# Kernel tuning notes

Measured on AMD Instinct MI355X. Metric: run time of the kernel, lower is better.

Reference implementation:

```python
import jax, jax.numpy as jnp
import numpy as np

V, E, H, S, B, T = 32000, 256, 512, 128, 32, 32


def setup_inputs() -> dict:
    key = jax.random.key(0)
    ks = iter(jax.random.split(key, 32))

    def w(shape, s=0.05):
        return jax.random.normal(next(ks), shape, dtype=jnp.float32) * s

    return dict(
        src=jax.random.randint(next(ks), (S, B), 0, V),
        trg=jax.random.randint(next(ks), (T, B), 0, V),
        embed=w((V, E)),
        enc_Wih_f=w((4 * H, E)), enc_Whh_f=w((4 * H, H)), enc_bih_f=w((4 * H,)), enc_bhh_f=w((4 * H,)),
        enc_Wih_b=w((4 * H, E)), enc_Whh_b=w((4 * H, H)), enc_bih_b=w((4 * H,)), enc_bhh_b=w((4 * H,)),
        attn_W=w((H, 2 * H)), attn_b=w((H,)), attn_v=w((H,)),
        dec_Wih0=w((4 * H, H + E)), dec_Whh0=w((4 * H, H)), dec_bih0=w((4 * H,)), dec_bhh0=w((4 * H,)),
        dec_Wih1=w((4 * H, H)), dec_Whh1=w((4 * H, H)), dec_bih1=w((4 * H,)), dec_bhh1=w((4 * H,)),
        out_W=w((V, 2 * H)), out_b=w((V,)),
    )


def _cell(x, h, c, Wih, Whh, bih, bhh):
    # PyTorch LSTM gate order: i, f, g, o
    z = x @ Wih.T + h @ Whh.T + bih + bhh
    i, f, g, o = jnp.split(z, 4, axis=-1)
    c2 = jax.nn.sigmoid(f) * c + jax.nn.sigmoid(i) * jnp.tanh(g)
    h2 = jax.nn.sigmoid(o) * jnp.tanh(c2)
    return h2, c2


def _run_lstm(xs, Wih, Whh, bih, bhh):
    # xs: [S, B, in]; returns outputs [S,B,H], final (h,c)
    h0 = jnp.zeros((xs.shape[1], Whh.shape[1]), xs.dtype)

    def step(carry, x):
        h, c = carry
        h2, c2 = _cell(x, h, c, Wih, Whh, bih, bhh)
        return (h2, c2), h2

    (hT, cT), outs = jax.lax.scan(step, (h0, h0), xs)
    return outs, hT, cT


def _forward(src, trg, embed,
             enc_Wih_f, enc_Whh_f, enc_bih_f, enc_bhh_f,
             enc_Wih_b, enc_Whh_b, enc_bih_b, enc_bhh_b,
             attn_W, attn_b, attn_v,
             dec_Wih0, dec_Whh0, dec_bih0, dec_bhh0,
             dec_Wih1, dec_Whh1, dec_bih1, dec_bhh1,
             out_W, out_b):
    emb_src = embed[src]                                  # [S,B,E]
    # bidirectional 1-layer encoder LSTM
    f_outs, hf, cf = _run_lstm(emb_src, enc_Wih_f, enc_Whh_f, enc_bih_f, enc_bhh_f)
    b_outs, hb, cb = _run_lstm(emb_src[::-1], enc_Wih_b, enc_Whh_b, enc_bih_b, enc_bhh_b)
    enc_out = f_outs + b_outs[::-1]                       # [S,B,H] (sum of directions)
    h = jnp.stack([hf, hb])                               # [2,B,H] -> decoder init state
    c = jnp.stack([cf, cb])
    enc_bsh = enc_out.transpose(1, 0, 2)                  # [B,S,H]

    def dec_step(carry, tok):
        h, c = carry
        emb = embed[tok]                                  # [B,E]
        q = h[-1]                                         # top-layer hidden [B,H]
        qs = jnp.broadcast_to(q[:, None, :], enc_bsh.shape)
        energy = jnp.tanh(jnp.concatenate([qs, enc_bsh], -1) @ attn_W.T + attn_b)  # [B,S,H]
        scores = energy @ attn_v                          # [B,S]
        aw = jax.nn.softmax(scores, axis=1)
        ctx = jnp.einsum('bs,bsh->bh', aw, enc_bsh)       # [B,H]
        x = jnp.concatenate([emb, ctx], -1)               # [B,E+H]
        h0, c0 = _cell(x, h[0], c[0], dec_Wih0, dec_Whh0, dec_bih0, dec_bhh0)
        h1, c1 = _cell(h0, h[1], c[1], dec_Wih1, dec_Whh1, dec_bih1, dec_bhh1)
        logits = jax.nn.log_softmax(
            jnp.concatenate([h1, ctx], -1) @ out_W.T + out_b, axis=-1)             # [B,V]
        return (jnp.stack([h0, h1]), jnp.stack([c0, c1])), logits

    # teacher forcing (ratio=1.0): input at step t is trg[t-1]
    _, outs = jax.lax.scan(dec_step, (h, c), trg[:-1])    # [T-1,B,V]
    outputs = jnp.concatenate(
        [jnp.zeros((1,) + outs.shape[1:], outs.dtype), outs], 0)  # outputs[0]=0 as in torch
    return outputs


def reference(src, trg, embed,
              enc_Wih_f, enc_Whh_f, enc_bih_f, enc_bhh_f,
              enc_Wih_b, enc_Whh_b, enc_bih_b, enc_bhh_b,
              attn_W, attn_b, attn_v,
              dec_Wih0, dec_Whh0, dec_bih0, dec_bhh0,
              dec_Wih1, dec_Whh1, dec_bih1, dec_bhh1,
              out_W, out_b):
    return _forward(src, trg, embed,
                    enc_Wih_f, enc_Whh_f, enc_bih_f, enc_bhh_f,
                    enc_Wih_b, enc_Whh_b, enc_bih_b, enc_bhh_b,
                    attn_W, attn_b, attn_v,
                    dec_Wih0, dec_Whh0, dec_bih0, dec_bhh0,
                    dec_Wih1, dec_Whh1, dec_bih1, dec_bhh1,
                    out_W, out_b)
```

## Files before the change

### kernel.cpp

```cpp
#include <hip/hip_runtime.h>
#include <stdint.h>


using short8 = __attribute__((ext_vector_type(8))) short;
using f32x4  = __attribute__((ext_vector_type(4))) float;
typedef _Float16 half2v __attribute__((ext_vector_type(2)));

__device__ __forceinline__ short f2bf(float x){
  unsigned u = __float_as_uint(x);
  unsigned r = (u + 0x7fffu + ((u >> 16) & 1u)) >> 16;
  return (short)(unsigned short)r;
}
__device__ __forceinline__ unsigned bfpair(float a, float b){
  return (unsigned)(unsigned short)f2bf(a) | ((unsigned)(unsigned short)f2bf(b) << 16);
}
__device__ __forceinline__ float bf2f_lo(unsigned u){ return __uint_as_float(u << 16); }
__device__ __forceinline__ float bf2f_hi(unsigned u){ return __uint_as_float(u & 0xffff0000u); }
__device__ __forceinline__ float sigmf(float x){ return 1.0f/(1.0f + __expf(-x)); }
__device__ __forceinline__ float fast_tanh(float x){
  const float e = __expf(2.0f*x);
  return 1.0f - 2.0f/(e + 1.0f);
}
__device__ __forceinline__ unsigned pack_h2(float a, float b){
  unsigned short ha = __builtin_bit_cast(unsigned short, (_Float16)a);
  unsigned short hb = __builtin_bit_cast(unsigned short, (_Float16)b);
  return (unsigned)ha | ((unsigned)hb << 16);
}
__device__ __forceinline__ float h2lo(unsigned u){ return (float)__builtin_bit_cast(half2v,u)[0]; }
__device__ __forceinline__ float h2hi(unsigned u){ return (float)__builtin_bit_cast(half2v,u)[1]; }
__device__ __forceinline__ float dot2u(unsigned x, unsigned w, float c){
#if __has_builtin(__builtin_amdgcn_fdot2)
  return __builtin_amdgcn_fdot2(__builtin_bit_cast(half2v,x), __builtin_bit_cast(half2v,w), c, false);
#else
  half2v hx = __builtin_bit_cast(half2v,x), hw = __builtin_bit_cast(half2v,w);
  c = fmaf((float)hx[0], (float)hw[0], c);
  c = fmaf((float)hx[1], (float)hw[1], c);
  return c;
#endif
}

__device__ __forceinline__ float4 load_coh_f4(const float* p){
  float4 v;
  asm volatile("global_load_dwordx4 %0, %1, off sc0 sc1\n\ts_waitcnt vmcnt(0)"
               : "=&v"(v) : "v"(p) : "memory");
  return v;
}
__device__ __forceinline__ void store_coh_u32(unsigned* p, unsigned v){
  asm volatile("global_store_dword %0, %1, off sc0 sc1" :: "v"(p), "v"(v) : "memory");
}
__device__ __forceinline__ void store_coh_f32(float* p, float v){
  asm volatile("global_store_dword %0, %1, off sc0 sc1" :: "v"(p), "v"(v) : "memory");
}

__device__ __forceinline__ void wait_cnt(const unsigned* base, unsigned target){
  if (threadIdx.x < 64){
    const bool mine = threadIdx.x < 8;
    const unsigned* p = base + (threadIdx.x << 4);
    for(;;){
      unsigned v = target;
      if (mine)
        asm volatile("global_load_dword %0, %1, off sc0 sc1\n\ts_waitcnt vmcnt(0)"
                     : "=&v"(v) : "v"(p) : "memory");
      if (__all(v >= target)) break;
    }
  }
  __syncthreads();
}
__device__ __forceinline__ void add0(unsigned* slot){
  if (threadIdx.x < 64) asm volatile("s_waitcnt vmcnt(0)" ::: "memory");
  if (threadIdx.x == 0)
    __hip_atomic_fetch_add(slot, 1u, __ATOMIC_RELAXED, __HIP_MEMORY_SCOPE_AGENT);
}

__device__ __forceinline__ void stage8u(const unsigned* src, int bg8, unsigned* lds){
  const unsigned* s0 = src + (size_t)bg8*2048;
  const int f0 = threadIdx.x, f1 = f0 + 256;
  uint4 a, b;
  asm volatile(
    "global_load_dwordx4 %0, %2, off sc0 sc1\n\t"
    "global_load_dwordx4 %1, %3, off sc0 sc1\n\t"
    "s_waitcnt vmcnt(0)"
    : "=&v"(a), "=&v"(b)
    : "v"(s0 + (f0<<2)), "v"(s0 + (f1<<2))
    : "memory");
  { const int row = f0>>6, cu = (f0&63)<<2; *(uint4*)&lds[row*260+cu] = a; }
  { const int row = f1>>6, cu = (f1&63)<<2; *(uint4*)&lds[row*260+cu] = b; }
}

__device__ __forceinline__ float dot512(const unsigned* xrow, const unsigned* w){
  float a = 0.f;
  #pragma unroll 4
  for (int it = 0; it < 16; ++it){
    uint4 x0 = *(const uint4*)(xrow + it*16);
    uint4 x1 = *(const uint4*)(xrow + it*16 + 4);
    uint4 x2 = *(const uint4*)(xrow + it*16 + 8);
    uint4 x3 = *(const uint4*)(xrow + it*16 + 12);
    uint4 w0 = *(const uint4*)(w + it*16);
    uint4 w1 = *(const uint4*)(w + it*16 + 4);
    uint4 w2 = *(const uint4*)(w + it*16 + 8);
    uint4 w3 = *(const uint4*)(w + it*16 + 12);
    a = dot2u(x0.x,w0.x,a); a = dot2u(x0.y,w0.y,a); a = dot2u(x0.z,w0.z,a); a = dot2u(x0.w,w0.w,a);
    a = dot2u(x1.x,w1.x,a); a = dot2u(x1.y,w1.y,a); a = dot2u(x1.z,w1.z,a); a = dot2u(x1.w,w1.w,a);
    a = dot2u(x2.x,w2.x,a); a = dot2u(x2.y,w2.y,a); a = dot2u(x2.z,w2.z,a); a = dot2u(x2.w,w2.w,a);
    a = dot2u(x3.x,w3.x,a); a = dot2u(x3.y,w3.y,a); a = dot2u(x3.z,w3.z,a); a = dot2u(x3.w,w3.w,a);
  }
  return a;
}

__device__ __forceinline__ float2 dot2rows(const unsigned* xrow, const unsigned* wA, const unsigned* wB){
  float a = 0.f, b = 0.f;
  #pragma unroll 8
  for (int it = 0; it < 32; ++it){
    uint4 x0 = *(const uint4*)(xrow + it*8);
    uint4 x1 = *(const uint4*)(xrow + it*8 + 4);
    uint4 a0 = *(const uint4*)(wA + it*8);
    uint4 a1 = *(const uint4*)(wA + it*8 + 4);
    uint4 b0 = *(const uint4*)(wB + it*8);
    uint4 b1 = *(const uint4*)(wB + it*8 + 4);
    a = dot2u(x0.x,a0.x,a); a = dot2u(x0.y,a0.y,a); a = dot2u(x0.z,a0.z,a); a = dot2u(x0.w,a0.w,a);
    a = dot2u(x1.x,a1.x,a); a = dot2u(x1.y,a1.y,a); a = dot2u(x1.z,a1.z,a); a = dot2u(x1.w,a1.w,a);
    b = dot2u(x0.x,b0.x,b); b = dot2u(x0.y,b0.y,b); b = dot2u(x0.z,b0.z,b); b = dot2u(x0.w,b0.w,b);
    b = dot2u(x1.x,b1.x,b); b = dot2u(x1.y,b1.y,b); b = dot2u(x1.w,b1.w,b); b = dot2u(x1.z,b1.z,b);
  }
  return make_float2(a, b);
}

__global__ void k_zero(float* __restrict__ p, int n){
  int i = blockIdx.x*256 + threadIdx.x;
  const int stride = gridDim.x*256;
  for (; i < n; i += stride) p[i] = 0.f;
}

__global__ __launch_bounds__(256) void k_cvt_f16(const float* __restrict__ s, unsigned short* __restrict__ d, int n){
  int i = blockIdx.x*256 + threadIdx.x;
  const int stride = gridDim.x*256;
  for (; i < n; i += stride) d[i] = __builtin_bit_cast(unsigned short, (_Float16)s[i]);
}
__global__ __launch_bounds__(256) void k_cvt_f16_str(const float* __restrict__ s, int lds_, unsigned short* __restrict__ d, int n){
  int i = blockIdx.x*256 + threadIdx.x;
  const int stride = gridDim.x*256;
  for (; i < n; i += stride){
    const int row = i >> 9, c = i & 511;
    d[i] = __builtin_bit_cast(unsigned short, (_Float16)s[(size_t)row*lds_ + c]);
  }
}

__global__ __launch_bounds__(256) void k_gather(
    const int* __restrict__ src, const int* __restrict__ trg,
    const float* __restrict__ embed,
    short* __restrict__ emb_src_bf, short* __restrict__ emb_trg_bf)
{
  const int row = blockIdx.x, tid = threadIdx.x;
  if (row < 4096){
    const int tok = src[row];
    emb_src_bf[(size_t)row*256 + tid] = f2bf(embed[(size_t)tok*256 + tid]);
  } else {
    const int r = row - 4096;
    short v = 0;
    if (r < 992){ const int tok = trg[r]; v = f2bf(embed[(size_t)tok*256 + tid]); }
    emb_trg_bf[(size_t)r*256 + tid] = v;
  }
}

__global__ __launch_bounds__(256) void k_gemm_aw(
    const short* __restrict__ A, int lda,
    const float* __restrict__ W, int ldw,
    float* __restrict__ C, int ldc,
    const float* __restrict__ bias0, const float* __restrict__ bias1,
    int Mvalid, int K, int tmode, short* __restrict__ Cbf)
{
  __shared__ __align__(16) short As[128*32];
  __shared__ __align__(16) short Bs[128*32];
  const int tid = threadIdx.x;
  const int bm = blockIdx.x, bn = blockIdx.y;
  const int w  = tid >> 6,  l  = tid & 63;
  const int wm = w >> 1,    wn = w & 1;
  const int lr = l & 15,    lk = l >> 4;

  const int r0 = tid >> 2;
  const int s0 = (tid & 3) << 3;
  const int r1 = r0 + 64;

  const short* a0 = A + (size_t)(bm*128 + r0)*lda + s0;
  const short* a1 = A + (size_t)(bm*128 + r1)*lda + s0;
  const float* w0 = W + (size_t)(bn*128 + r0)*ldw + s0;
  const float* w1 = W + (size_t)(bn*128 + r1)*ldw + s0;

  const f32x4 zero4 = {0.f,0.f,0.f,0.f};
  f32x4 acc[4][4];
  #pragma unroll
  for (int mi=0;mi<4;mi++){
    #pragma unroll
    for (int ni=0;ni<4;ni++) acc[mi][ni] = zero4;
  }

  for (int k0 = 0; k0 < K; k0 += 32){
    short8 va0 = *(const short8*)(a0 + k0);
    short8 va1 = *(const short8*)(a1 + k0);
    float4 f00 = *(const float4*)(w0 + k0);
    float4 f01 = *(const float4*)(w0 + k0 + 4);
    float4 f10 = *(const float4*)(w1 + k0);
    float4 f11 = *(const float4*)(w1 + k0 + 4);
    short8 vb0, vb1;
    vb0[0]=f2bf(f00.x); vb0[1]=f2bf(f00.y); vb0[2]=f2bf(f00.z); vb0[3]=f2bf(f00.w);
    vb0[4]=f2bf(f01.x); vb0[5]=f2bf(f01.y); vb0[6]=f2bf(f01.z); vb0[7]=f2bf(f01.w);
    vb1[0]=f2bf(f10.x); vb1[1]=f2bf(f10.y); vb1[2]=f2bf(f10.z); vb1[3]=f2bf(f10.w);
    vb1[4]=f2bf(f11.x); vb1[5]=f2bf(f11.y); vb1[6]=f2bf(f11.z); vb1[7]=f2bf(f11.w);

    __syncthreads();
    *((short8*)As + tid)       = va0;
    *((short8*)As + tid + 256) = va1;
    *((short8*)Bs + tid)       = vb0;
    *((short8*)Bs + tid + 256) = vb1;
    __syncthreads();

    short8 af[4], bfr[4];
    #pragma unroll
    for (int mi=0;mi<4;mi++) af[mi]  = *(const short8*)&As[(wm*64 + mi*16 + lr)*32 + (lk<<3)];
    #pragma unroll
    for (int ni=0;ni<4;ni++) bfr[ni] = *(const short8*)&Bs[(wn*64 + ni*16 + lr)*32 + (lk<<3)];
    #pragma unroll
    for (int mi=0;mi<4;mi++){
      #pragma unroll
      for (int ni=0;ni<4;ni++)
        acc[mi][ni] = __builtin_amdgcn_mfma_f32_16x16x32_bf16(af[mi], bfr[ni], acc[mi][ni], 0,0,0);
    }
  }

  #pragma unroll
  for (int mi=0;mi<4;mi++){
    const int rb = bm*128 + wm*64 + mi*16 + (lk<<2);
    #pragma unroll
    for (int ni=0;ni<4;ni++){
      const int col = bn*128 + wn*64 + ni*16 + lr;
      float bv = 0.f;
      if (bias0) bv += bias0[col];
      if (bias1) bv += bias1[col];
      #pragma unroll
      for (int rr=0;rr<4;rr++){
        const int row = rb + rr;
        if (row < Mvalid){
          const float vv = acc[mi][ni][rr] + bv;
          if (Cbf)        Cbf[(size_t)row*ldc + col] = f2bf(vv);
          else if (tmode) C[(size_t)(row>>5)*65536 + (size_t)col*32 + (row&31)] = vv;
          else            C[(size_t)row*ldc + col] = vv;
        }
      }
    }
  }
}

__global__ __launch_bounds__(256,1) void k_enc_persist(
    const float* __restrict__ pre_f, const float* __restrict__ pre_b,
    const unsigned short* __restrict__ WhF, const unsigned short* __restrict__ WhB,
    unsigned* __restrict__ f_outs, unsigned* __restrict__ b_outs,
    float* __restrict__ c_f_out, float* __restrict__ c_b_out,
    unsigned* __restrict__ encCnt)
{
  __shared__ __align__(16) unsigned x_lds[8*260];
  __shared__ float zbuf[64*8];
  const int bid = blockIdx.x, tid = threadIdx.x;
  const int x = bid & 7, m = bid >> 3;
  const int dir = m & 1, bg = (m >> 1) & 3, q = m >> 3;
  const int jb = x*4 + q;
  const float* pre = dir ? pre_b : pre_f;
  const unsigned* Wh = (const unsigned*)(dir ? WhB : WhF);
  unsigned* outs = dir ? b_outs : f_outs;
  float* c_out = dir ? c_b_out : c_f_out;
  unsigned* grp = encCnt + (size_t)(dir*4 + bg)*128;
  unsigned* mycnt = grp + x*16;

  const int bb = tid & 7, rr = tid >> 3;
  const int g = rr >> 3, op = rr & 7;
  const unsigned* wA = Wh + (size_t)(g*512 + jb*16 + 2*op)*256;
  const unsigned* wB = wA + 256;

  const int cp = tid & 7, fb = tid >> 3;
  const int b_out = bg*8 + fb;
  const int k0 = jb*16 + 2*cp;
  float c_a = 0.f, c_b2 = 0.f;

  for (int t = 0; t < 128; ++t){
    float pz[8];
    if (tid < 64){
      const int tt = dir ? (127 - t) : t;
      const float* pt = pre + (size_t)tt*65536;
      #pragma unroll
      for (int gg = 0; gg < 4; ++gg){
        pz[gg]   = pt[(size_t)(gg*512 + k0)*32 + b_out];
        pz[gg+4] = pt[(size_t)(gg*512 + k0 + 1)*32 + b_out];
      }
    }
    if (t){
      wait_cnt(grp, 4u*(unsigned)t);
      stage8u(outs + (size_t)(t-1)*8192, bg, x_lds);
    } else {
      for (int i = tid; i < 8*260; i += 256) x_lds[i] = 0;
    }
    __syncthreads();

    const float2 d = dot2rows(x_lds + bb*260, wA, wB);
    zbuf[(g*16 + 2*op)*8 + bb]   = d.x;
    zbuf[(g*16 + 2*op+1)*8 + bb] = d.y;
    __syncthreads();

    if (tid < 64){
      float za[4], zb[4];
      #pragma unroll
      for (int gg = 0; gg < 4; ++gg){
        za[gg] = pz[gg]   + zbuf[(gg*16 + 2*cp)*8 + fb];
        zb[gg] = pz[gg+4] + zbuf[(gg*16 + 2*cp+1)*8 + fb];
      }
      const float ca = sigmf(za[1])*c_a  + sigmf(za[0])*fast_tanh(za[2]);
      const float cb = sigmf(zb[1])*c_b2 + sigmf(zb[0])*fast_tanh(zb[2]);
      c_a = ca; c_b2 = cb;
      const float ha = sigmf(za[3])*fast_tanh(ca);
      const float hb = sigmf(zb[3])*fast_tanh(cb);
      store_coh_u32(outs + (size_t)t*8192 + (size_t)b_out*256 + (k0>>1), pack_h2(ha, hb));
    }
    add0(mycnt);
  }
  if (tid < 64){
    c_out[b_out*512 + k0]     = c_a;
    c_out[b_out*512 + k0 + 1] = c_b2;
  }
}

__global__ __launch_bounds__(256) void k_sum_enc(
    const unsigned* __restrict__ f_o, const unsigned* __restrict__ b_o,
    unsigned* __restrict__ enc_sum_bf_u)
{
  const int i = blockIdx.x*256 + threadIdx.x;
  const int s = i >> 13, rem = i & 8191;
  const unsigned a = f_o[i], b = b_o[(size_t)(127 - s)*8192 + rem];
  const float lo = h2lo(a) + h2lo(b);
  const float hi = h2hi(a) + h2hi(b);
  enc_sum_bf_u[i] = bfpair(lo, hi);
}

__global__ __launch_bounds__(256,1) void k_dec_persist(
    const float* __restrict__ demb,
    const unsigned short* __restrict__ Wih0h,
    const unsigned short* __restrict__ Whh0h,
    const unsigned short* __restrict__ Wih1h,
    const unsigned short* __restrict__ Whh1h,
    const float* __restrict__ bih1, const float* __restrict__ bhh1,
    const unsigned short* __restrict__ wqh,
    const float* __restrict__ attnV,
    const short* __restrict__ enc_proj_bf,
    const unsigned* __restrict__ enc_sum_u,
    const unsigned* __restrict__ h0i, const unsigned* __restrict__ h1i,
    const float* __restrict__ c0_init, const float* __restrict__ c1_init,
    unsigned* __restrict__ h0buf, unsigned* __restrict__ h1buf,
    unsigned* __restrict__ ctxb,
    float* __restrict__ qsb,
    short* __restrict__ h1ctx,
    unsigned* __restrict__ cE1, unsigned* __restrict__ cE2,
    unsigned* __restrict__ cE3, unsigned* __restrict__ cE4)
{
  __shared__ __align__(16) unsigned x1s[8*260];
  __shared__ __align__(16) unsigned x0s[8*260];
  __shared__ float zfin[32*9];
  __shared__ __align__(16) float q_s[512], v_s[512];
  __shared__ float part[256], aw[128], red[128];

  const int bid = blockIdx.x, tid = threadIdx.x;
  const int x = bid & 7;
  const int bg = (bid >> 3) & 3;
  const int q = bid >> 5;
  const int jb = x*8 + q;

  unsigned* e1 = cE1 + bg*128;
  unsigned* e2 = cE2 + bg*128;
  unsigned* e3 = cE3 + bg*128;
  unsigned* e4 = cE4 + bg*128;

  const int b = tid & 7, r = tid >> 3;
  const int g = r >> 3, o = r & 7;
  const int j_row = g*512 + jb*8 + o;

  const int cp = tid & 3, fb = tid >> 2;
  const int b_out = bg*8 + fb;
  const int k0 = jb*8 + 2*cp;

  const unsigned* Wh0row = (const unsigned*)Whh0h + (size_t)j_row*256;
  const unsigned* Wh1row = (const unsigned*)Whh1h + (size_t)j_row*256;
  const unsigned* Wi0row = (const unsigned*)Wih0h + (size_t)j_row*256;
  const unsigned* Wi1row = (const unsigned*)Wih1h + (size_t)j_row*256;

  float c0a = 0.f, c0b = 0.f, c1a = 0.f, c1b = 0.f;
  float b1a[4], b1b[4];
  if (tid < 32){
    c0a = c0_init[b_out*512 + k0];   c0b = c0_init[b_out*512 + k0 + 1];
    c1a = c1_init[b_out*512 + k0];   c1b = c1_init[b_out*512 + k0 + 1];
    #pragma unroll
    for (int gg=0; gg<4; ++gg){
      b1a[gg] = bih1[gg*512 + k0]     + bhh1[gg*512 + k0];
      b1b[gg] = bih1[gg*512 + k0 + 1] + bhh1[gg*512 + k0 + 1];
    }
  }
  if (bid < 32 && tid < 128) ((float4*)v_s)[tid] = ((const float4*)attnV)[tid];

  float zh0 = 0.f;

  for (int t = 0; t < 31; ++t){
    const float demb_v = demb[(size_t)t*65536 + (size_t)j_row*32 + bg*8 + b];

    if (t){
      wait_cnt(e4, 8u*(unsigned)t);
      stage8u(h1buf + (size_t)(t&1)*8192, bg, x1s);
    } else {
      stage8u(h1i, bg, x1s);
      stage8u(h0i, bg, x0s);
    }
    __syncthreads();
    if (t == 0) zh0 = dot512(x0s + b*260, Wh0row);
    const float zh1 = dot512(x1s + b*260, Wh1row);
    if (tid < 64){
      const int qb = tid >> 3, qcol = jb*8 + (tid & 7);
      const float qv = dot512(x1s + qb*260, (const unsigned*)wqh + (size_t)qcol*256);
      store_coh_f32(qsb + (size_t)(bg*8 + qb)*512 + qcol, qv);
    }
    add0(e1 + x*16);

    if (bid < 32){
      wait_cnt(e1, 8u*(unsigned)(t+1));
      const int ab = bid;
      if (tid < 128) ((float4*)q_s)[tid] = load_coh_f4(qsb + (size_t)ab*512 + (tid<<2));
      __syncthreads();
      {
        const int s = tid >> 1, half = tid & 1;
        const unsigned* ep = (const unsigned*)(enc_proj_bf + ((size_t)(s*32 + ab))*512 + (half << 8));
        const float* qh = q_s + (half << 8);
        const float* vh = v_s + (half << 8);
        float p = 0.f;
        for (int kk = 0; kk < 128; kk += 4){
          uint4 e = *(const uint4*)(ep + kk);
          const int k2 = kk << 1;
          p += fast_tanh(qh[k2+0] + bf2f_lo(e.x)) * vh[k2+0];
          p += fast_tanh(qh[k2+1] + bf2f_hi(e.x)) * vh[k2+1];
          p += fast_tanh(qh[k2+2] + bf2f_lo(e.y)) * vh[k2+2];
          p += fast_tanh(qh[k2+3] + bf2f_hi(e.y)) * vh[k2+3];
          p += fast_tanh(qh[k2+4] + bf2f_lo(e.z)) * vh[k2+4];
          p += fast_tanh(qh[k2+5] + bf2f_hi(e.z)) * vh[k2+5];
          p += fast_tanh(qh[k2+6] + bf2f_lo(e.w)) * vh[k2+6];
          p += fast_tanh(qh[k2+7] + bf2f_hi(e.w)) * vh[k2+7];
        }
        part[tid] = p;
      }
      __syncthreads();
      if (tid < 128){ const float sc = part[2*tid] + part[2*tid+1]; aw[tid] = sc; red[tid] = sc; }
      __syncthreads();
      for (int off = 64; off > 0; off >>= 1){
        if (tid < off) red[tid] = fmaxf(red[tid], red[tid+off]);
        __syncthreads();
      }
      const float mx = red[0];
      __syncthreads();
      if (tid < 128){ const float e = __expf(aw[tid] - mx); aw[tid] = e; red[tid] = e; }
      __syncthreads();
      for (int off = 64; off > 0; off >>= 1){
        if (tid < off) red[tid] += red[tid+off];
        __syncthreads();
      }
      const float inv = 1.0f / red[0];
      if (tid < 128) aw[tid] *= inv;
      __syncthreads();
      if (tid < 64){
        const unsigned* es = enc_sum_u + (size_t)ab*256 + (tid<<2);
        float c0=0,c1=0,c2=0,c3=0,c4=0,c5=0,c6=0,c7=0;
        for (int s2 = 0; s2 < 128; ++s2){
          const float a = aw[s2];
          uint4 u = *(const uint4*)(es + (size_t)s2*8192);
          c0 = fmaf(a, bf2f_lo(u.x), c0); c1 = fmaf(a, bf2f_hi(u.x), c1);
          c2 = fmaf(a, bf2f_lo(u.y), c2); c3 = fmaf(a, bf2f_hi(u.y), c3);
          c4 = fmaf(a, bf2f_lo(u.z), c4); c5 = fmaf(a, bf2f_hi(u.z), c5);
          c6 = fmaf(a, bf2f_lo(u.w), c6); c7 = fmaf(a, bf2f_hi(u.w), c7);
        }
        unsigned* cp4 = ctxb + (size_t)ab*256 + (tid<<2);
        store_coh_u32(cp4+0, pack_h2(c0,c1));
        store_coh_u32(cp4+1, pack_h2(c2,c3));
        store_coh_u32(cp4+2, pack_h2(c4,c5));
        store_coh_u32(cp4+3, pack_h2(c6,c7));
        unsigned* hc = (unsigned*)h1ctx + ((size_t)t*16384 + (size_t)ab*512 + 256 + (tid<<2));
        hc[0] = bfpair(c0,c1); hc[1] = bfpair(c2,c3); hc[2] = bfpair(c4,c5); hc[3] = bfpair(c6,c7);
      }
      add0(e2 + (bid & 7)*16);
    }

    wait_cnt(e2, (unsigned)(t+1));
    stage8u(ctxb, bg, x0s);
    __syncthreads();
    zfin[r*9 + b] = demb_v + dot512(x0s + b*260, Wi0row) + zh0;
    __syncthreads();
    if (tid < 32){
      float za[4], zb[4];
      #pragma unroll
      for (int gg=0; gg<4; ++gg){
        za[gg] = zfin[(gg*8 + 2*cp)*9 + fb];
        zb[gg] = zfin[(gg*8 + 2*cp+1)*9 + fb];
      }
      const float ca = sigmf(za[1])*c0a + sigmf(za[0])*fast_tanh(za[2]);
      const float cb = sigmf(zb[1])*c0b + sigmf(zb[0])*fast_tanh(zb[2]);
      c0a = ca; c0b = cb;
      const float ha = sigmf(za[3])*fast_tanh(ca);
      const float hb = sigmf(zb[3])*fast_tanh(cb);
      store_coh_u32(h0buf + (size_t)((t+1)&1)*8192 + (size_t)b_out*256 + (k0>>1), pack_h2(ha, hb));
    }
    add0(e3 + x*16);

    wait_cnt(e3, 8u*(unsigned)(t+1));
    stage8u(h0buf + (size_t)((t+1)&1)*8192, bg, x1s);
    __syncthreads();
    {
      const float2 d = dot2rows(x1s + b*260, Wi1row, Wh0row);
      zfin[r*9 + b] = d.x + zh1;
      zh0 = d.y;
    }
    __syncthreads();
    if (tid < 32){
      float za[4], zb[4];
      #pragma unroll
      for (int gg=0; gg<4; ++gg){
        za[gg] = b1a[gg] + zfin[(gg*8 + 2*cp)*9 + fb];
        zb[gg] = b1b[gg] + zfin[(gg*8 + 2*cp+1)*9 + fb];
      }
      const float ca = sigmf(za[1])*c1a + sigmf(za[0])*fast_tanh(za[2]);
      const float cb = sigmf(zb[1])*c1b + sigmf(zb[0])*fast_tanh(zb[2]);
      c1a = ca; c1b = cb;
      const float ha = sigmf(za[3])*fast_tanh(ca);
      const float hb = sigmf(zb[3])*fast_tanh(cb);
      store_coh_u32(h1buf + (size_t)((t+1)&1)*8192 + (size_t)b_out*256 + (k0>>1), pack_h2(ha, hb));
      ((unsigned*)h1ctx)[(size_t)t*16384 + (size_t)b_out*512 + (k0>>1)] = bfpair(ha, hb);
    }
    add0(e4 + x*16);
  }
}

__global__ __launch_bounds__(256) void k_logsm(float* __restrict__ out){
  float* row = out + (size_t)blockIdx.x * 32000;
  const int tid = threadIdx.x;
  __shared__ float red[256];
  float s = 0.f;
  for (int i = tid; i < 8000; i += 256){
    const float4 v = ((const float4*)row)[i];
    s += __expf(v.x) + __expf(v.y) + __expf(v.z) + __expf(v.w);
  }
  red[tid] = s; __syncthreads();
  for (int off = 128; off > 0; off >>= 1){
    if (tid < off) red[tid] += red[tid+off];
    __syncthreads();
  }
  const float lse = __logf(red[0]);
  for (int i = tid; i < 8000; i += 256){
    float4 v = ((const float4*)row)[i];
    v.x -= lse; v.y -= lse; v.z -= lse; v.w -= lse;
    ((float4*)row)[i] = v;
  }
}

extern "C" void kernel_launch(void* const* d_in, const int* in_sizes, int n_in,
                              void* d_out, int out_size, void* d_ws, size_t ws_size,
                              hipStream_t stream)
{
  (void)in_sizes; (void)n_in; (void)out_size; (void)ws_size;
  const int*   src   = (const int*)d_in[0];
  const int*   trg   = (const int*)d_in[1];
  const float* embed = (const float*)d_in[2];
  const float* eWihF = (const float*)d_in[3];
  const float* eWhhF = (const float*)d_in[4];
  const float* ebihF = (const float*)d_in[5];
  const float* ebhhF = (const float*)d_in[6];
  const float* eWihB = (const float*)d_in[7];
  const float* eWhhB = (const float*)d_in[8];
  const float* ebihB = (const float*)d_in[9];
  const float* ebhhB = (const float*)d_in[10];
  const float* attnW = (const float*)d_in[11];
  const float* attnB = (const float*)d_in[12];
  const float* attnV = (const float*)d_in[13];
  const float* dWih0 = (const float*)d_in[14];
  const float* dWhh0 = (const float*)d_in[15];
  const float* dbih0 = (const float*)d_in[16];
  const float* dbhh0 = (const float*)d_in[17];
  const float* dWih1 = (const float*)d_in[18];
  const float* dWhh1 = (const float*)d_in[19];
  const float* dbih1 = (const float*)d_in[20];
  const float* dbhh1 = (const float*)d_in[21];
  const float* outW  = (const float*)d_in[22];
  const float* outB  = (const float*)d_in[23];

  float* out = (float*)d_out;
  float* enc_in_f = out;
  float* enc_in_b = out + 8388608;
  short* enc_proj_bf = (short*)(out + 18874368);
  unsigned* f_outs = (unsigned*)(out + 20971520);
  unsigned* b_outs = (unsigned*)(out + 23068672);
  float* demb     = out + 25165824;
  short* emb_src_bf = (short*)(out + 27262976);
  short* emb_trg_bf = (short*)(out + 27787264);
  unsigned* enc_sum_bf_u = (unsigned*)(out + 27918336);
  unsigned short* wqh    = (unsigned short*)(out + 28966912);
  unsigned short* whhF_h = (unsigned short*)(out + 29229056);
  unsigned short* whhB_h = (unsigned short*)(out + 29753344);
  unsigned short* wih0_h = (unsigned short*)(out + 30277632);
  unsigned short* whh0_h = (unsigned short*)(out + 30801920);
  unsigned short* wih1_h = (unsigned short*)(out + 31326208);
  unsigned short* whh1_h = (unsigned short*)(out + 31850496);
  float* qsb            = out + 32374784;

  char* ws = (char*)d_ws;
  short* h1ctx = (short*)ws;
  unsigned* h0buf = (unsigned*)(ws + 2097152);
  unsigned* h1buf = (unsigned*)(ws + 2162688);
  unsigned* ctxb  = (unsigned*)(ws + 2228224);
  float* c_f      = (float*)(ws + 2260992);
  float* c_b      = (float*)(ws + 2326528);
  unsigned* encCnt = (unsigned*)(ws + 2392064);
  unsigned* cE1    = encCnt + 1024;
  unsigned* cE2    = cE1 + 512;
  unsigned* cE3    = cE2 + 512;
  unsigned* cE4    = cE3 + 512;

  k_zero<<<2, 256, 0, stream>>>((float*)encCnt, 3072);
  k_gather<<<5120, 256, 0, stream>>>(src, trg, embed, emb_src_bf, emb_trg_bf);
  {
    dim3 g1(32,16);
    k_gemm_aw<<<g1,256,0,stream>>>(emb_src_bf,256, eWihF,256, enc_in_f,2048, ebihF,ebhhF, 4096,256, 1, nullptr);
    k_gemm_aw<<<g1,256,0,stream>>>(emb_src_bf,256, eWihB,256, enc_in_b,2048, ebihB,ebhhB, 4096,256, 1, nullptr);
    dim3 g2(8,16);
    k_gemm_aw<<<g2,256,0,stream>>>(emb_trg_bf,256, dWih0,768, demb,2048, dbih0,dbhh0, 1024,256, 1, nullptr);
  }
  k_cvt_f16<<<1024,256,0,stream>>>(eWhhF, whhF_h, 1048576);
  k_cvt_f16<<<1024,256,0,stream>>>(eWhhB, whhB_h, 1048576);
  k_cvt_f16_str<<<1024,256,0,stream>>>(dWih0+256, 768, wih0_h, 1048576);
  k_cvt_f16<<<1024,256,0,stream>>>(dWhh0, whh0_h, 1048576);
  k_cvt_f16<<<1024,256,0,stream>>>(dWih1, wih1_h, 1048576);
  k_cvt_f16<<<1024,256,0,stream>>>(dWhh1, whh1_h, 1048576);
  k_cvt_f16_str<<<256,256,0,stream>>>(attnW, 1024, wqh, 262144);
  k_enc_persist<<<256, 256, 0, stream>>>(enc_in_f, enc_in_b, whhF_h, whhB_h,
                                         f_outs, b_outs, c_f, c_b, encCnt);
  k_sum_enc<<<4096, 256, 0, stream>>>(f_outs, b_outs, enc_sum_bf_u);
  {
    dim3 g3(32,4);
    k_gemm_aw<<<g3,256,0,stream>>>((const short*)enc_sum_bf_u,512, attnW+512,1024, nullptr,512, attnB,nullptr, 4096,512, 0, enc_proj_bf);
  }
  k_dec_persist<<<256, 256, 0, stream>>>(demb, wih0_h, whh0_h, wih1_h, whh1_h,
                                         dbih1, dbhh1, wqh, attnV, enc_proj_bf,
                                         enc_sum_bf_u,
                                         f_outs + (size_t)127*8192, b_outs + (size_t)127*8192,
                                         c_f, c_b, h0buf, h1buf, ctxb, qsb, h1ctx,
                                         cE1, cE2, cE3, cE4);
  k_zero<<<512, 256, 0, stream>>>(out, 1024000);
  {
    dim3 g4(8,250);
    k_gemm_aw<<<g4,256,0,stream>>>(h1ctx,1024, outW,1024, out + 1024000, 32000, outB,nullptr, 992,1024, 0, nullptr);
  }
  k_logsm<<<992, 256, 0, stream>>>(out + 1024000);
}
```

Measured before the change: 2.429 ms.

## Replace counter-based grid barriers with sentinel-polled per-timestep buffers

The persistent encoder and decoder kernels stop using atomic arrival counters and wait_cnt spin barriers. Producers now write into per-timestep buffers that were prefilled with a sentinel value, and consumers poll the data itself until no sentinel remains. This removes the atomic-then-poll round trip and the block-wide barrier on every recurrent step. The cost is extra fill kernels and larger buffers. Correctness now depends on the 0x7FFF7FFF pattern (two f16 NaNs, or a NaN float) never appearing as a real value.

Result: slower. 2.665 ms (+9.7%).

```diff
diff --git a/kernel.cpp b/kernel.cpp
--- a/kernel.cpp
+++ b/kernel.cpp
@@ -5,6 +5,8 @@
 using short8 = __attribute__((ext_vector_type(8))) short;
 using f32x4  = __attribute__((ext_vector_type(4))) float;
 typedef _Float16 half2v __attribute__((ext_vector_type(2)));
+
+#define SENT 0x7FFF7FFFu
 
 __device__ __forceinline__ short f2bf(float x){
   unsigned u = __float_as_uint(x);
@@ -39,37 +41,11 @@
 #endif
 }
 
-__device__ __forceinline__ float4 load_coh_f4(const float* p){
-  float4 v;
-  asm volatile("global_load_dwordx4 %0, %1, off sc0 sc1\n\ts_waitcnt vmcnt(0)"
-               : "=&v"(v) : "v"(p) : "memory");
-  return v;
-}
 __device__ __forceinline__ void store_coh_u32(unsigned* p, unsigned v){
   asm volatile("global_store_dword %0, %1, off sc0 sc1" :: "v"(p), "v"(v) : "memory");
 }
 __device__ __forceinline__ void store_coh_f32(float* p, float v){
   asm volatile("global_store_dword %0, %1, off sc0 sc1" :: "v"(p), "v"(v) : "memory");
-}
-
-__device__ __forceinline__ void wait_cnt(const unsigned* base, unsigned target){
-  if (threadIdx.x < 64){
-    const bool mine = threadIdx.x < 8;
-    const unsigned* p = base + (threadIdx.x << 4);
-    for(;;){
-      unsigned v = target;
-      if (mine)
-        asm volatile("global_load_dword %0, %1, off sc0 sc1\n\ts_waitcnt vmcnt(0)"
-                     : "=&v"(v) : "v"(p) : "memory");
-      if (__all(v >= target)) break;
-    }
-  }
-  __syncthreads();
-}
-__device__ __forceinline__ void add0(unsigned* slot){
-  if (threadIdx.x < 64) asm volatile("s_waitcnt vmcnt(0)" ::: "memory");
-  if (threadIdx.x == 0)
-    __hip_atomic_fetch_add(slot, 1u, __ATOMIC_RELAXED, __HIP_MEMORY_SCOPE_AGENT);
 }
 
 __device__ __forceinline__ void stage8u(const unsigned* src, int bg8, unsigned* lds){
@@ -83,6 +59,25 @@
     : "=&v"(a), "=&v"(b)
     : "v"(s0 + (f0<<2)), "v"(s0 + (f1<<2))
     : "memory");
+  { const int row = f0>>6, cu = (f0&63)<<2; *(uint4*)&lds[row*260+cu] = a; }
+  { const int row = f1>>6, cu = (f1&63)<<2; *(uint4*)&lds[row*260+cu] = b; }
+}
+
+__device__ __forceinline__ void stage8p(const unsigned* src, int bg8, unsigned* lds){
+  const unsigned* s0 = src + (size_t)bg8*2048;
+  const int f0 = threadIdx.x, f1 = f0 + 256;
+  const unsigned* p0 = s0 + (f0<<2);
+  const unsigned* p1 = s0 + (f1<<2);
+  uint4 a, b;
+  for(;;){
+    asm volatile(
+      "global_load_dwordx4 %0, %2, off sc0 sc1\n\t"
+      "global_load_dwordx4 %1, %3, off sc0 sc1\n\t"
+      "s_waitcnt vmcnt(0)"
+      : "=&v"(a), "=&v"(b) : "v"(p0), "v"(p1) : "memory");
+    if (a.x!=SENT && a.y!=SENT && a.z!=SENT && a.w!=SENT &&
+        b.x!=SENT && b.y!=SENT && b.z!=SENT && b.w!=SENT) break;
+  }
   { const int row = f0>>6, cu = (f0&63)<<2; *(uint4*)&lds[row*260+cu] = a; }
   { const int row = f1>>6, cu = (f1&63)<<2; *(uint4*)&lds[row*260+cu] = b; }
 }
@@ -129,6 +124,11 @@
   int i = blockIdx.x*256 + threadIdx.x;
   const int stride = gridDim.x*256;
   for (; i < n; i += stride) p[i] = 0.f;
+}
+__global__ void k_fill(unsigned* __restrict__ p, int n, unsigned v){
+  int i = blockIdx.x*256 + threadIdx.x;
+  const int stride = gridDim.x*256;
+  for (; i < n; i += stride) p[i] = v;
 }
 
 __global__ __launch_bounds__(256) void k_cvt_f16(const float* __restrict__ s, unsigned short* __restrict__ d, int n){
@@ -254,8 +254,7 @@
     const float* __restrict__ pre_f, const float* __restrict__ pre_b,
     const unsigned short* __restrict__ WhF, const unsigned short* __restrict__ WhB,
     unsigned* __restrict__ f_outs, unsigned* __restrict__ b_outs,
-    float* __restrict__ c_f_out, float* __restrict__ c_b_out,
-    unsigned* __restrict__ encCnt)
+    float* __restrict__ c_f_out, float* __restrict__ c_b_out)
 {
   __shared__ __align__(16) unsigned x_lds[8*260];
   __shared__ float zbuf[64*8];
@@ -267,8 +266,6 @@
   const unsigned* Wh = (const unsigned*)(dir ? WhB : WhF);
   unsigned* outs = dir ? b_outs : f_outs;
   float* c_out = dir ? c_b_out : c_f_out;
-  unsigned* grp = encCnt + (size_t)(dir*4 + bg)*128;
-  unsigned* mycnt = grp + x*16;
 
   const int bb = tid & 7, rr = tid >> 3;
   const int g = rr >> 3, op = rr & 7;
@@ -292,8 +289,7 @@
       }
     }
     if (t){
-      wait_cnt(grp, 4u*(unsigned)t);
-      stage8u(outs + (size_t)(t-1)*8192, bg, x_lds);
+      stage8p(outs + (size_t)(t-1)*8192, bg, x_lds);
     } else {
       for (int i = tid; i < 8*260; i += 256) x_lds[i] = 0;
     }
@@ -318,7 +314,6 @@
       const float hb = sigmf(zb[3])*fast_tanh(cb);
       store_coh_u32(outs + (size_t)t*8192 + (size_t)b_out*256 + (k0>>1), pack_h2(ha, hb));
     }
-    add0(mycnt);
   }
   if (tid < 64){
     c_out[b_out*512 + k0]     = c_a;
@@ -351,12 +346,11 @@
     const unsigned* __restrict__ enc_sum_u,
     const unsigned* __restrict__ h0i, const unsigned* __restrict__ h1i,
     const float* __restrict__ c0_init, const float* __restrict__ c1_init,
-    unsigned* __restrict__ h0buf, unsigned* __restrict__ h1buf,
-    unsigned* __restrict__ ctxb,
-    float* __restrict__ qsb,
-    short* __restrict__ h1ctx,
-    unsigned* __restrict__ cE1, unsigned* __restrict__ cE2,
-    unsigned* __restrict__ cE3, unsigned* __restrict__ cE4)
+    float* __restrict__ qs_t,
+    unsigned* __restrict__ h0t,
+    unsigned* __restrict__ h1t,
+    unsigned* __restrict__ ctxt,
+    short* __restrict__ h1ctx)
 {
   __shared__ __align__(16) unsigned x1s[8*260];
   __shared__ __align__(16) unsigned x0s[8*260];
@@ -369,11 +363,7 @@
   const int bg = (bid >> 3) & 3;
   const int q = bid >> 5;
   const int jb = x*8 + q;
-
-  unsigned* e1 = cE1 + bg*128;
-  unsigned* e2 = cE2 + bg*128;
-  unsigned* e3 = cE3 + bg*128;
-  unsigned* e4 = cE4 + bg*128;
+  (void)x;
 
   const int b = tid & 7, r = tid >> 3;
   const int g = r >> 3, o = r & 7;
@@ -407,8 +397,7 @@
     const float demb_v = demb[(size_t)t*65536 + (size_t)j_row*32 + bg*8 + b];
 
     if (t){
-      wait_cnt(e4, 8u*(unsigned)t);
-      stage8u(h1buf + (size_t)(t&1)*8192, bg, x1s);
+      stage8p(h1t + (size_t)(t-1)*8192, bg, x1s);
     } else {
       stage8u(h1i, bg, x1s);
       stage8u(h0i, bg, x0s);
@@ -419,14 +408,21 @@
     if (tid < 64){
       const int qb = tid >> 3, qcol = jb*8 + (tid & 7);
       const float qv = dot512(x1s + qb*260, (const unsigned*)wqh + (size_t)qcol*256);
-      store_coh_f32(qsb + (size_t)(bg*8 + qb)*512 + qcol, qv);
-    }
-    add0(e1 + x*16);
+      store_coh_f32(qs_t + (size_t)t*16384 + (size_t)(bg*8 + qb)*512 + qcol, qv);
+    }
 
     if (bid < 32){
-      wait_cnt(e1, 8u*(unsigned)(t+1));
       const int ab = bid;
-      if (tid < 128) ((float4*)q_s)[tid] = load_coh_f4(qsb + (size_t)ab*512 + (tid<<2));
+      if (tid < 128){
+        const unsigned* p = (const unsigned*)(qs_t + (size_t)t*16384 + (size_t)ab*512) + (tid<<2);
+        uint4 v;
+        for(;;){
+          asm volatile("global_load_dwordx4 %0, %1, off sc0 sc1\n\ts_waitcnt vmcnt(0)"
+                       : "=&v"(v) : "v"(p) : "memory");
+          if (v.x!=SENT && v.y!=SENT && v.z!=SENT && v.w!=SENT) break;
+        }
+        ((uint4*)q_s)[tid] = v;
+      }
       __syncthreads();
       {
         const int s = tid >> 1, half = tid & 1;
@@ -477,7 +473,7 @@
           c4 = fmaf(a, bf2f_lo(u.z), c4); c5 = fmaf(a, bf2f_hi(u.z), c5);
           c6 = fmaf(a, bf2f_lo(u.w), c6); c7 = fmaf(a, bf2f_hi(u.w), c7);
         }
-        unsigned* cp4 = ctxb + (size_t)ab*256 + (tid<<2);
+        unsigned* cp4 = ctxt + (size_t)t*8192 + (size_t)ab*256 + (tid<<2);
         store_coh_u32(cp4+0, pack_h2(c0,c1));
         store_coh_u32(cp4+1, pack_h2(c2,c3));
         store_coh_u32(cp4+2, pack_h2(c4,c5));
@@ -485,11 +481,9 @@
         unsigned* hc = (unsigned*)h1ctx + ((size_t)t*16384 + (size_t)ab*512 + 256 + (tid<<2));
         hc[0] = bfpair(c0,c1); hc[1] = bfpair(c2,c3); hc[2] = bfpair(c4,c5); hc[3] = bfpair(c6,c7);
       }
-      add0(e2 + (bid & 7)*16);
-    }
-
-    wait_cnt(e2, (unsigned)(t+1));
-    stage8u(ctxb, bg, x0s);
+    }
+
+    stage8p(ctxt + (size_t)t*8192, bg, x0s);
     __syncthreads();
     zfin[r*9 + b] = demb_v + dot512(x0s + b*260, Wi0row) + zh0;
     __syncthreads();
@@ -505,12 +499,10 @@
       c0a = ca; c0b = cb;
       const float ha = sigmf(za[3])*fast_tanh(ca);
       const float hb = sigmf(zb[3])*fast_tanh(cb);
-      store_coh_u32(h0buf + (size_t)((t+1)&1)*8192 + (size_t)b_out*256 + (k0>>1), pack_h2(ha, hb));
-    }
-    add0(e3 + x*16);
-
-    wait_cnt(e3, 8u*(unsigned)(t+1));
-    stage8u(h0buf + (size_t)((t+1)&1)*8192, bg, x1s);
+      store_coh_u32(h0t + (size_t)t*8192 + (size_t)b_out*256 + (k0>>1), pack_h2(ha, hb));
+    }
+
+    stage8p(h0t + (size_t)t*8192, bg, x1s);
     __syncthreads();
     {
       const float2 d = dot2rows(x1s + b*260, Wi1row, Wh0row);
@@ -530,10 +522,9 @@
       c1a = ca; c1b = cb;
       const float ha = sigmf(za[3])*fast_tanh(ca);
       const float hb = sigmf(zb[3])*fast_tanh(cb);
-      store_coh_u32(h1buf + (size_t)((t+1)&1)*8192 + (size_t)b_out*256 + (k0>>1), pack_h2(ha, hb));
+      store_coh_u32(h1t + (size_t)t*8192 + (size_t)b_out*256 + (k0>>1), pack_h2(ha, hb));
       ((unsigned*)h1ctx)[(size_t)t*16384 + (size_t)b_out*512 + (k0>>1)] = bfpair(ha, hb);
     }
-    add0(e4 + x*16);
   }
 }
 
@@ -592,6 +583,10 @@
   float* out = (float*)d_out;
   float* enc_in_f = out;
   float* enc_in_b = out + 8388608;
+  float* qs_t     = out + 16777216;
+  unsigned* h0t   = (unsigned*)(out + 17285120);
+  unsigned* h1t   = (unsigned*)(out + 17539072);
+  unsigned* ctxt  = (unsigned*)(out + 17793024);
   short* enc_proj_bf = (short*)(out + 18874368);
   unsigned* f_outs = (unsigned*)(out + 20971520);
   unsigned* b_outs = (unsigned*)(out + 23068672);
@@ -606,22 +601,15 @@
   unsigned short* whh0_h = (unsigned short*)(out + 30801920);
   unsigned short* wih1_h = (unsigned short*)(out + 31326208);
   unsigned short* whh1_h = (unsigned short*)(out + 31850496);
-  float* qsb            = out + 32374784;
 
   char* ws = (char*)d_ws;
   short* h1ctx = (short*)ws;
-  unsigned* h0buf = (unsigned*)(ws + 2097152);
-  unsigned* h1buf = (unsigned*)(ws + 2162688);
-  unsigned* ctxb  = (unsigned*)(ws + 2228224);
-  float* c_f      = (float*)(ws + 2260992);
-  float* c_b      = (float*)(ws + 2326528);
-  unsigned* encCnt = (unsigned*)(ws + 2392064);
-  unsigned* cE1    = encCnt + 1024;
-  unsigned* cE2    = cE1 + 512;
-  unsigned* cE3    = cE2 + 512;
-  unsigned* cE4    = cE3 + 512;
-
-  k_zero<<<2, 256, 0, stream>>>((float*)encCnt, 3072);
+  float* c_f   = (float*)(ws + 2097152);
+  float* c_b   = (float*)(ws + 2162688);
+
+  k_fill<<<512, 256, 0, stream>>>((unsigned*)qs_t, 1269760, SENT);
+  k_fill<<<512, 256, 0, stream>>>(f_outs, 1048576, SENT);
+  k_fill<<<512, 256, 0, stream>>>(b_outs, 1048576, SENT);
   k_gather<<<5120, 256, 0, stream>>>(src, trg, embed, emb_src_bf, emb_trg_bf);
   {
     dim3 g1(32,16);
@@ -638,7 +626,7 @@
   k_cvt_f16<<<1024,256,0,stream>>>(dWhh1, whh1_h, 1048576);
   k_cvt_f16_str<<<256,256,0,stream>>>(attnW, 1024, wqh, 262144);
   k_enc_persist<<<256, 256, 0, stream>>>(enc_in_f, enc_in_b, whhF_h, whhB_h,
-                                         f_outs, b_outs, c_f, c_b, encCnt);
+                                         f_outs, b_outs, c_f, c_b);
   k_sum_enc<<<4096, 256, 0, stream>>>(f_outs, b_outs, enc_sum_bf_u);
   {
     dim3 g3(32,4);
@@ -648,8 +636,7 @@
                                          dbih1, dbhh1, wqh, attnV, enc_proj_bf,
                                          enc_sum_bf_u,
                                          f_outs + (size_t)127*8192, b_outs + (size_t)127*8192,
-                                         c_f, c_b, h0buf, h1buf, ctxb, qsb, h1ctx,
-                                         cE1, cE2, cE3, cE4);
+                                         c_f, c_b, qs_t, h0t, h1t, ctxt, h1ctx);
   k_zero<<<512, 256, 0, stream>>>(out, 1024000);
   {
     dim3 g4(8,250);
```
